# Kernel tuning notes

Hardware: AMD Instinct MI355X
Metric: run time of the kernel (lower is better)

Reference implementation:

```python
import jax, jax.numpy as jnp
import numpy as np
from functools import reduce

N_QUBITS = 6
DIM = 2 ** N_QUBITS  # 64

# PauliZ expectation signs per wire: zsign[j, q] = +1 if bit q of basis state j is 0 else -1
# PennyLane convention: wire 0 is the most-significant bit.
_ZSIGN = jnp.asarray(1.0 - 2.0 * ((np.arange(DIM)[:, None] >> (N_QUBITS - 1 - np.arange(N_QUBITS))[None, :]) & 1), dtype=jnp.float32)  # [64, 6]

def _cnot_perm(c, t):
    # permutation p with new_state[j] = old_state[p[j]] for CNOT(control=c, target=t)
    idx = np.arange(DIM)
    cbit = (idx >> (N_QUBITS - 1 - c)) & 1
    return idx ^ (cbit << (N_QUBITS - 1 - t))

def _ring_perm(r):
    # compose the ring of CNOTs: CNOT(w, (w+r)%n) for w = 0..n-1 applied in order
    total = np.arange(DIM)
    for w in range(N_QUBITS):
        total = total[_cnot_perm(w, (w + r) % N_QUBITS)]
    return total

_RING = {r: jnp.asarray(_ring_perm(r)) for r in (1, 2)}

def _rot(phi, theta, omega):
    # PennyLane Rot(phi, theta, omega) = RZ(omega) @ RY(theta) @ RZ(phi)
    c = jnp.cos(theta / 2.0)
    s = jnp.sin(theta / 2.0)
    em = jnp.exp(-0.5j * (phi + omega))
    ep = jnp.exp(0.5j * (phi - omega))
    return jnp.stack([jnp.stack([em * c, -ep * s]),
                      jnp.stack([jnp.conj(ep) * s, jnp.conj(em) * c])])

def _strongly_entangling(psi, theta):
    # theta: [L, N_QUBITS, 3]; psi: [B, 64] complex
    L = theta.shape[0]
    for l in range(L):
        mats = [_rot(theta[l, w, 0], theta[l, w, 1], theta[l, w, 2]) for w in range(N_QUBITS)]
        U = reduce(jnp.kron, mats)  # [64, 64]; wire 0 = most significant, matches kron order
        psi = psi @ U.T
        r = l % (N_QUBITS - 1) + 1  # PennyLane default ranges
        psi = psi[:, _RING[r]]
    return psi

def setup_inputs() -> dict:
    key = jax.random.key(0)
    ks = jax.random.split(key, 12)
    B, D, H, NW = 131072, 64, 64, 5
    return {
        'x': jax.random.normal(ks[0], (B, D), dtype=jnp.float32),
        'W1': jax.random.normal(ks[1], (H, D), dtype=jnp.float32) * 0.1,
        'b1': jnp.zeros((H,), dtype=jnp.float32),
        'ln_g': jnp.ones((H,), dtype=jnp.float32),
        'ln_b': jnp.zeros((H,), dtype=jnp.float32),
        'W2': jax.random.normal(ks[2], (N_QUBITS, H), dtype=jnp.float32) * 0.1,
        'b2': jnp.zeros((N_QUBITS,), dtype=jnp.float32),
        'theta_shared': jax.random.normal(ks[3], (2, N_QUBITS, 3), dtype=jnp.float32) * 0.1,
        'theta_task': jax.random.normal(ks[4], (1, N_QUBITS, 3), dtype=jnp.float32) * 0.1,
        'Wc': jax.random.normal(ks[5], (NW, N_QUBITS), dtype=jnp.float32) * 0.1,
        'bc': jnp.zeros((NW,), dtype=jnp.float32),
    }

def reference(x, W1, b1, ln_g, ln_b, W2, b2, theta_shared, theta_task, Wc, bc):
    # --- encoder: Linear -> ReLU -> LayerNorm -> Linear -> Tanh ---
    h = jax.nn.relu(x @ W1.T + b1)
    mu = h.mean(-1, keepdims=True)
    var = ((h - mu) ** 2).mean(-1, keepdims=True)
    h = (h - mu) / jnp.sqrt(var + 1e-5) * ln_g + ln_b
    z = jnp.tanh(h @ W2.T + b2)  # [B, 6], in [-1, 1]
    # --- amplitude prep: RY(pi * z_q) on |0> per qubit -> product state ---
    half = (jnp.pi * z) / 2.0
    vec = jnp.stack([jnp.cos(half), jnp.sin(half)], axis=-1)  # [B, 6, 2]
    psi = vec[:, 0]
    for q in range(1, N_QUBITS):
        psi = (psi[:, :, None] * vec[:, q][:, None, :]).reshape(psi.shape[0], -1)
    psi = psi.astype(jnp.complex64)  # [B, 64]
    # --- VQC layers ---
    psi = _strongly_entangling(psi, theta_shared)
    psi = _strongly_entangling(psi, theta_task)
    # --- PauliZ expectation per wire ---
    probs = (psi * jnp.conj(psi)).real  # [B, 64]
    q_out = probs @ _ZSIGN  # [B, 6]
    # --- linear classifier ---
    return q_out @ Wc.T + bc
```

## Files before the change

### kernel.cpp

```cpp
#include <hip/hip_runtime.h>
#include <utility>

#define NQ 6
#define DIM 64

typedef float v2f __attribute__((ext_vector_type(2)));

namespace {

constexpr int ring_entry(int r, int i) {
    int idx = i;
    for (int w = NQ - 1; w >= 0; --w) {
        int c = w;
        int t = (w + r) % NQ;
        int cbit = (idx >> (NQ - 1 - c)) & 1;
        idx ^= cbit << (NQ - 1 - t);
    }
    return idx;
}

constexpr int Mc(int L, int i) {
    if (L == 1) return ring_entry(1, i);
    if (L == 2) return ring_entry(1, ring_entry(2, i));
    if (L == 3) return ring_entry(1, ring_entry(2, ring_entry(1, i)));
    return i;
}

constexpr int Minv(int L, int p) {
    for (int i = 0; i < DIM; ++i) if (Mc(L, i) == p) return i;
    return -1;
}

}

__device__ __forceinline__ float swap1(float v) {
    return __int_as_float(__builtin_amdgcn_mov_dpp(__float_as_int(v), 0xB1, 0xF, 0xF, true));
}
__device__ __forceinline__ v2f swap1v(v2f v) {
    v2f r; r.x = swap1(v.x); r.y = swap1(v.y); return r;
}
__device__ __forceinline__ v2f nsw(v2f v) {
    v2f r; r.x = -v.y; r.y = v.x; return r;
}


template<int LY, int W, int d, int... Ls>
__device__ __forceinline__ void wire_inlane(v2f* sv,
        float A0r, float A0i, float B0r, float B0i,
        float A1r, float A1i, float B1r, float B1i,
        std::integer_sequence<int, Ls...>) {
    (([&] {
        if constexpr (Ls < (Ls ^ d)) {
            constexpr int la = Ls, lb = Ls ^ d;
            constexpr int ra = (Minv(LY, la) >> (5 - W)) & 1;
            constexpr int rb = (Minv(LY, lb) >> (5 - W)) & 1;
            const float cAar = ra ? A1r : A0r, cAai = ra ? A1i : A0i;
            const float cBar = ra ? B1r : B0r, cBai = ra ? B1i : B0i;
            const float cAbr = rb ? A1r : A0r, cAbi = rb ? A1i : A0i;
            const float cBbr = rb ? B1r : B0r, cBbi = rb ? B1i : B0i;
            const v2f ma = sv[la], mb = sv[lb];
            const v2f na = nsw(ma), nb = nsw(mb);
            sv[la] = cAar*ma + cAai*na + cBar*mb + cBai*nb;
            sv[lb] = cAbr*mb + cAbi*nb + cBbr*ma + cBbi*na;
        }
    }()), ...);
}

template<int LY, int W, int... Ls>
__device__ __forceinline__ void wire_cross0(v2f* sv,
        float A0r, float A0i, float B0r, float B0i,
        float A1r, float A1i, float B1r, float B1i,
        std::integer_sequence<int, Ls...>) {
    (([&] {
        constexpr int r = (Minv(LY, Ls) >> (5 - W)) & 1;
        const float cAr = r ? A1r : A0r, cAi = r ? A1i : A0i;
        const float cBr = r ? B1r : B0r, cBi = r ? B1i : B0i;
        const v2f m = sv[Ls];
        const v2f t = swap1v(m);
        sv[Ls] = cAr*m + cAi*nsw(m) + cBr*t + cBi*nsw(t);
    }()), ...);
}

template<int LY, int W, int d, int... Ls>
__device__ __forceinline__ void wire_crossd(v2f* sv,
        float A0r, float A0i, float B0r, float B0i,
        float A1r, float A1i, float B1r, float B1i,
        std::integer_sequence<int, Ls...>) {
    (([&] {
        if constexpr (Ls < (Ls ^ d)) {
            constexpr int la = Ls, lb = Ls ^ d;
            constexpr int ra = (Minv(LY, la) >> (5 - W)) & 1;
            constexpr int rb = (Minv(LY, lb) >> (5 - W)) & 1;
            const float cAar = ra ? A1r : A0r, cAai = ra ? A1i : A0i;
            const float cBar = ra ? B1r : B0r, cBai = ra ? B1i : B0i;
            const float cAbr = rb ? A1r : A0r, cAbi = rb ? A1i : A0i;
            const float cBbr = rb ? B1r : B0r, cBbi = rb ? B1i : B0i;
            const v2f ma = sv[la], mb = sv[lb];
            const v2f ta = swap1v(mb);
            const v2f tb = swap1v(ma);
            sv[la] = cAar*ma + cAai*nsw(ma) + cBar*ta + cBai*nsw(ta);
            sv[lb] = cAbr*mb + cAbi*nsw(mb) + cBbr*tb + cBbi*nsw(tb);
        }
    }()), ...);
}

template<int LY, int W>
__device__ __forceinline__ void wire_apply(v2f* sv,
        const float* __restrict__ g, bool par) {
    constexpr int D = Mc(LY, 1 << (5 - W));
    constexpr bool cross = (D >> 5) & 1;
    constexpr int d = D & 31;
    constexpr bool cpar = (Minv(LY, 32) >> (5 - W)) & 1;

    float A0r, A0i, B0r, B0i, A1r, A1i, B1r, B1i;
    if constexpr (cpar) {
        A0r = par ? g[6] : g[0];  A0i = par ? g[7] : g[1];
        B0r = par ? g[4] : g[2];  B0i = par ? g[5] : g[3];
        A1r = par ? g[0] : g[6];  A1i = par ? g[1] : g[7];
        B1r = par ? g[2] : g[4];  B1i = par ? g[3] : g[5];
    } else {
        A0r = g[0]; A0i = g[1]; B0r = g[2]; B0i = g[3];
        A1r = g[6]; A1i = g[7]; B1r = g[4]; B1i = g[5];
    }
    if constexpr (!cross) {
        wire_inlane<LY, W, d>(sv, A0r, A0i, B0r, B0i, A1r, A1i, B1r, B1i,
                              std::make_integer_sequence<int, 32>{});
    } else if constexpr (d == 0) {
        wire_cross0<LY, W>(sv, A0r, A0i, B0r, B0i, A1r, A1i, B1r, B1i,
                           std::make_integer_sequence<int, 32>{});
    } else {
        wire_crossd<LY, W, d>(sv, A0r, A0i, B0r, B0i, A1r, A1i, B1r, B1i,
                              std::make_integer_sequence<int, 32>{});
    }
}

template<int LY>
__device__ __forceinline__ void layer_apply(v2f* sv,
        const float* __restrict__ g, bool par) {
    wire_apply<LY, 0>(sv, g,      par);
    wire_apply<LY, 1>(sv, g + 8,  par);
    wire_apply<LY, 2>(sv, g + 16, par);
    wire_apply<LY, 3>(sv, g + 24, par);
    wire_apply<LY, 4>(sv, g + 32, par);
    wire_apply<LY, 5>(sv, g + 40, par);
}

template<int... Ls>
__device__ __forceinline__ void readout_impl(const v2f* sv, float* q,
                                             std::integer_sequence<int, Ls...>) {
    (([&] {
        constexpr int iv = Minv(3, Ls);
        const float pb = fmaf(sv[Ls].x, sv[Ls].x, sv[Ls].y * sv[Ls].y);
        q[0] += ((iv >> 5) & 1) ? -pb : pb;
        q[1] += ((iv >> 4) & 1) ? -pb : pb;
        q[2] += ((iv >> 3) & 1) ? -pb : pb;
        q[3] += ((iv >> 2) & 1) ? -pb : pb;
        q[4] += ((iv >> 1) & 1) ? -pb : pb;
        q[5] += ( iv       & 1) ? -pb : pb;
    }()), ...);
}

__device__ __forceinline__ void compute_gates6(const float* __restrict__ th, float* g) {
#pragma unroll
    for (int w = 0; w < NQ; ++w) {
        const float phi = th[w*3+0], theta = th[w*3+1], omega = th[w*3+2];
        float s, c, sa, ca, sb, cb;
        __sincosf(0.5f * theta, &s, &c);
        __sincosf(0.5f * (phi + omega), &sa, &ca);
        __sincosf(0.5f * (phi - omega), &sb, &cb);
        g[w*8+0] =  ca * c;  g[w*8+1] = -sa * c;
        g[w*8+2] = -cb * s;  g[w*8+3] = -sb * s;
        g[w*8+4] =  cb * s;  g[w*8+5] = -sb * s;
        g[w*8+6] =  ca * c;  g[w*8+7] =  sa * c;
    }
}

__global__ void setup_kernel(const float* __restrict__ th_s, const float* __restrict__ th_t,
                             const float* __restrict__ ln_g, const float* __restrict__ ln_b,
                             const float* __restrict__ W2, const float* __restrict__ b2,
                             float* __restrict__ ws) {
    const int t = threadIdx.x;
    if (t < 18) {
        const int l = t / 6, w = t % 6;
        const float* th = (l < 2) ? (th_s + (l * 6 + w) * 3) : (th_t + w * 3);
        const float phi = th[0], theta = th[1], omega = th[2];
        float s, c, sa, ca, sb, cb;
        sincosf(0.5f * theta, &s, &c);
        sincosf(0.5f * (phi + omega), &sa, &ca);
        sincosf(0.5f * (phi - omega), &sb, &cb);
        float* g = ws + t * 8;
        g[0] =  ca * c;  g[1] = -sa * c;
        g[2] = -cb * s;  g[3] = -sb * s;
        g[4] =  cb * s;  g[5] = -sb * s;
        g[6] =  ca * c;  g[7] =  sa * c;
    }
    if (t < 384) {
        const int j = t / 6, m = t % 6;
        ws[144 + t] = ln_g[j] * W2[m * 64 + j];
    }
    if (t < 6) {
        float c1 = 0.f, c2 = 0.f;
        for (int j = 0; j < 64; ++j) {
            c1 += ln_g[j] * W2[t * 64 + j];
            c2 += ln_b[j] * W2[t * 64 + j];
        }
        ws[528 + t] = c1;
        ws[534 + t] = c2 + b2[t];
    }
}

template<bool USE_WS>
__global__ __launch_bounds__(256, 4)
void qmaml_kernel(
    const float* __restrict__ x,  const float* __restrict__ W1, const float* __restrict__ b1,
    const float* __restrict__ ln_g, const float* __restrict__ ln_b,
    const float* __restrict__ W2, const float* __restrict__ b2,
    const float* __restrict__ th_s, const float* __restrict__ th_t,
    const float* __restrict__ Wc, const float* __restrict__ bc,
    const float* __restrict__ ws, float* __restrict__ out, int nrows) {

    __shared__ float4 wl[1024];
    {
        const float4* wg = (const float4*)W1;
        const int tid = threadIdx.x;
#pragma unroll
        for (int k = 0; k < 4; ++k) wl[tid + (k << 8)] = wg[tid + (k << 8)];
    }
    __syncthreads();

    const int t   = blockIdx.x * 256 + threadIdx.x;
    const int row = t >> 1;
    const bool par = t & 1;
    if (row >= nrows) return;

    float4 xv[8];
    const float4* xp = (const float4*)(x + (long)row * 64 + par * 32);
#pragma unroll
    for (int k = 0; k < 8; ++k) xv[k] = xp[k];
    v2f xl[16];
#pragma unroll
    for (int k = 0; k < 8; ++k) {
        xl[2*k].x   = xv[k].x; xl[2*k].y   = xv[k].y;
        xl[2*k+1].x = xv[k].z; xl[2*k+1].y = xv[k].w;
    }

    v2f A2[3]; A2[0] = 0.f; A2[1] = 0.f; A2[2] = 0.f;
    float A[6]  = {0.f, 0.f, 0.f, 0.f, 0.f, 0.f};
    float C1[6] = {0.f, 0.f, 0.f, 0.f, 0.f, 0.f};
    float C2[6] = {0.f, 0.f, 0.f, 0.f, 0.f, 0.f};
    float s = 0.f, s2 = 0.f;

    const float4* whalf = &wl[par * 8];
#pragma unroll 2
    for (int j = 0; j < 64; ++j) {
        const float4* wr = whalf + j * 16;
        v2f pa; pa = 0.f;
        v2f pb; pb = 0.f;
#pragma unroll
        for (int k = 0; k < 8; k += 2) {
            const float4 a4 = wr[k];
            const float4 b4 = wr[k + 1];
            v2f w0; w0.x = a4.x; w0.y = a4.y;
            v2f w1; w1.x = a4.z; w1.y = a4.w;
            v2f w2v; w2v.x = b4.x; w2v.y = b4.y;
            v2f w3; w3.x = b4.z; w3.y = b4.w;
            pa = w0  * xl[2*k]     + pa;
            pb = w1  * xl[2*k + 1] + pb;
            pa = w2v * xl[2*k + 2] + pa;
            pb = w3  * xl[2*k + 3] + pb;
        }
        const v2f pv = pa + pb;
        const float p   = pv.x + pv.y;
        const float tot = p + swap1(p);
        const float acc = fmaxf(tot + b1[j], 0.f);
        s += acc; s2 = fmaf(acc, acc, s2);
        if constexpr (USE_WS) {
            const v2f* Gt2 = (const v2f*)(ws + 144 + j * 6);
            A2[0] = acc * Gt2[0] + A2[0];
            A2[1] = acc * Gt2[1] + A2[1];
            A2[2] = acc * Gt2[2] + A2[2];
        } else {
            const float gj = ln_g[j], bj = ln_b[j];
#pragma unroll
            for (int m = 0; m < 6; ++m) {
                const float w2 = W2[m * 64 + j];
                const float gw = gj * w2;
                A[m]  = fmaf(acc, gw, A[m]);
                C1[m] += gw;
                C2[m] = fmaf(bj, w2, C2[m]);
            }
        }
    }
    if constexpr (USE_WS) {
        A[0] = A2[0].x; A[1] = A2[0].y; A[2] = A2[1].x;
        A[3] = A2[1].y; A[4] = A2[2].x; A[5] = A2[2].y;
    }

    const float mu  = s  * (1.f / 64.f);
    const float var = s2 * (1.f / 64.f) - mu * mu;
    const float inv = rsqrtf(var + 1e-5f);

    float vc[6], vsn[6];
#pragma unroll
    for (int m = 0; m < 6; ++m) {
        float c1v, c2v;
        if constexpr (USE_WS) { c1v = ws[528 + m]; c2v = ws[534 + m]; }
        else                  { c1v = C1[m];       c2v = C2[m] + b2[m]; }
        const float zp = inv * (A[m] - mu * c1v) + c2v;
        const float e  = __expf(2.f * zp);
        const float z  = 1.f - 2.f / (e + 1.f);
        const float half = 1.57079632679f * z;
        vsn[m] = __sinf(half);
        vc[m]  = __cosf(half);
    }

    float gf[48];
    const float* g0;
    if constexpr (USE_WS) g0 = ws;
    else { compute_gates6(th_s, gf); g0 = gf; }

    v2f sv[32];
    {
        const float a0r = par ? (g0[4]*vc[0] + g0[6]*vsn[0]) : (g0[0]*vc[0] + g0[2]*vsn[0]);
        const float a0i = par ? (g0[5]*vc[0] + g0[7]*vsn[0]) : (g0[1]*vc[0] + g0[3]*vsn[0]);
        v2f ga1; ga1.x = g0[8]  * vc[1] + g0[10] * vsn[1];
                 ga1.y = g0[9]  * vc[1] + g0[11] * vsn[1];
        v2f gb1; gb1.x = g0[12] * vc[1] + g0[14] * vsn[1];
                 gb1.y = g0[13] * vc[1] + g0[15] * vsn[1];
        sv[0] = a0r * ga1 + a0i * nsw(ga1);
        sv[1] = a0r * gb1 + a0i * nsw(gb1);
    }
    {
        v2f ya; ya.x = g0[16]*vc[2] + g0[18]*vsn[2]; ya.y = g0[17]*vc[2] + g0[19]*vsn[2];
        v2f yb; yb.x = g0[20]*vc[2] + g0[22]*vsn[2]; yb.y = g0[21]*vc[2] + g0[23]*vsn[2];
        const v2f nya = nsw(ya), nyb = nsw(yb);
#pragma unroll
        for (int k = 3; k >= 0; --k) {
            const v2f h = sv[k >> 1];
            const v2f y  = (k & 1) ? yb  : ya;
            const v2f ny = (k & 1) ? nyb : nya;
            sv[k] = h.x * y + h.y * ny;
        }
    }
    {
        v2f ya; ya.x = g0[24]*vc[3] + g0[26]*vsn[3]; ya.y = g0[25]*vc[3] + g0[27]*vsn[3];
        v2f yb; yb.x = g0[28]*vc[3] + g0[30]*vsn[3]; yb.y = g0[29]*vc[3] + g0[31]*vsn[3];
        const v2f nya = nsw(ya), nyb = nsw(yb);
#pragma unroll
        for (int k = 7; k >= 0; --k) {
            const v2f h = sv[k >> 1];
            const v2f y  = (k & 1) ? yb  : ya;
            const v2f ny = (k & 1) ? nyb : nya;
            sv[k] = h.x * y + h.y * ny;
        }
    }
    {
        v2f ya; ya.x = g0[32]*vc[4] + g0[34]*vsn[4]; ya.y = g0[33]*vc[4] + g0[35]*vsn[4];
        v2f yb; yb.x = g0[36]*vc[4] + g0[38]*vsn[4]; yb.y = g0[37]*vc[4] + g0[39]*vsn[4];
        const v2f nya = nsw(ya), nyb = nsw(yb);
#pragma unroll
        for (int k = 15; k >= 0; --k) {
            const v2f h = sv[k >> 1];
            const v2f y  = (k & 1) ? yb  : ya;
            const v2f ny = (k & 1) ? nyb : nya;
            sv[k] = h.x * y + h.y * ny;
        }
    }
    {
        v2f ya; ya.x = g0[40]*vc[5] + g0[42]*vsn[5]; ya.y = g0[41]*vc[5] + g0[43]*vsn[5];
        v2f yb; yb.x = g0[44]*vc[5] + g0[46]*vsn[5]; yb.y = g0[45]*vc[5] + g0[47]*vsn[5];
        const v2f nya = nsw(ya), nyb = nsw(yb);
#pragma unroll
        for (int k = 31; k >= 0; --k) {
            const v2f h = sv[k >> 1];
            const v2f y  = (k & 1) ? yb  : ya;
            const v2f ny = (k & 1) ? nyb : nya;
            sv[k] = h.x * y + h.y * ny;
        }
    }

    if constexpr (USE_WS) {
        layer_apply<1>(sv, ws + 48, par);
        layer_apply<2>(sv, ws + 96, par);
    } else {
        compute_gates6(th_s + 18, gf);
        layer_apply<1>(sv, gf, par);
        compute_gates6(th_t, gf);
        layer_apply<2>(sv, gf, par);
    }

    float q[6] = {0.f, 0.f, 0.f, 0.f, 0.f, 0.f};
    readout_impl(sv, q, std::make_integer_sequence<int, 32>{});

    const float pm = par ? -1.f : 1.f;
    constexpr int invC = Minv(3, 32);
#pragma unroll
    for (int w = 0; w < 6; ++w) {
        float tq = q[w];
        if ((invC >> (5 - w)) & 1) tq *= pm;
        q[w] = tq + swap1(tq);
    }

    float o[5];
#pragma unroll
    for (int n = 0; n < 5; ++n) {
        float v = bc[n];
#pragma unroll
        for (int w = 0; w < 6; ++w) v = fmaf(q[w], Wc[n * 6 + w], v);
        o[n] = v;
    }
    float* orow = out + (long)row * 5;
    if (!par) { orow[0] = o[0]; orow[1] = o[1]; orow[2] = o[2]; }
    else      { orow[3] = o[3]; orow[4] = o[4]; }
}

extern "C" void kernel_launch(void* const* d_in, const int* in_sizes, int n_in,
                              void* d_out, int out_size, void* d_ws, size_t ws_size,
                              hipStream_t stream) {
    const float* x   = (const float*)d_in[0];
    const float* W1  = (const float*)d_in[1];
    const float* b1  = (const float*)d_in[2];
    const float* lng = (const float*)d_in[3];
    const float* lnb = (const float*)d_in[4];
    const float* W2  = (const float*)d_in[5];
    const float* b2  = (const float*)d_in[6];
    const float* ths = (const float*)d_in[7];
    const float* tht = (const float*)d_in[8];
    const float* Wc  = (const float*)d_in[9];
    const float* bc  = (const float*)d_in[10];
    float* out = (float*)d_out;
    float* ws  = (float*)d_ws;

    const int nrows = in_sizes[0] / 64;
    const int nthreads = nrows * 2;
    const int grid = (nthreads + 255) / 256;

    if (ws_size >= 540 * sizeof(float)) {
        setup_kernel<<<1, 384, 0, stream>>>(ths, tht, lng, lnb, W2, b2, ws);
        qmaml_kernel<true><<<grid, 256, 0, stream>>>(x, W1, b1, lng, lnb, W2, b2,
                                                     ths, tht, Wc, bc, ws, out, nrows);
    } else {
        qmaml_kernel<false><<<grid, 256, 0, stream>>>(x, W1, b1, lng, lnb, W2, b2,
                                                      ths, tht, Wc, bc, nullptr, out, nrows);
    }
}
```

Measured before the change: 140.6 us.

## Split hidden units across thread pair instead of input dimension

Measured after the change: 147.1 us. 1.05x slower.

```diff
diff --git a/kernel.cpp b/kernel.cpp
--- a/kernel.cpp
+++ b/kernel.cpp
@@ -178,7 +178,7 @@
 __global__ void setup_kernel(const float* __restrict__ th_s, const float* __restrict__ th_t,
                              const float* __restrict__ ln_g, const float* __restrict__ ln_b,
                              const float* __restrict__ W2, const float* __restrict__ b2,
-                             float* __restrict__ ws) {
+                             const float* __restrict__ b1, float* __restrict__ ws) {
     const int t = threadIdx.x;
     if (t < 18) {
         const int l = t / 6, w = t % 6;
@@ -196,7 +196,11 @@
     }
     if (t < 384) {
         const int j = t / 6, m = t % 6;
-        ws[144 + t] = ln_g[j] * W2[m * 64 + j];
+        ws[144 + j * 8 + m] = ln_g[j] * W2[m * 64 + j];
+    }
+    if (t < 64) {
+        ws[144 + t * 8 + 6] = b1[t];
+        ws[144 + t * 8 + 7] = 0.f;
     }
     if (t < 6) {
         float c1 = 0.f, c2 = 0.f;
@@ -204,8 +208,8 @@
             c1 += ln_g[j] * W2[t * 64 + j];
             c2 += ln_b[j] * W2[t * 64 + j];
         }
-        ws[528 + t] = c1;
-        ws[534 + t] = c2 + b2[t];
+        ws[656 + t] = c1;
+        ws[662 + t] = c2 + b2[t];
     }
 }
 
@@ -233,15 +237,15 @@
     const bool par = t & 1;
     if (row >= nrows) return;
 
-    float4 xv[8];
-    const float4* xp = (const float4*)(x + (long)row * 64 + par * 32);
-#pragma unroll
-    for (int k = 0; k < 8; ++k) xv[k] = xp[k];
-    v2f xl[16];
-#pragma unroll
-    for (int k = 0; k < 8; ++k) {
-        xl[2*k].x   = xv[k].x; xl[2*k].y   = xv[k].y;
-        xl[2*k+1].x = xv[k].z; xl[2*k+1].y = xv[k].w;
+    v2f xl[32];
+    {
+        const float4* xp = (const float4*)(x + (long)row * 64);
+#pragma unroll
+        for (int k = 0; k < 16; ++k) {
+            const float4 v = xp[k];
+            xl[2*k].x   = v.x; xl[2*k].y   = v.y;
+            xl[2*k+1].x = v.z; xl[2*k+1].y = v.w;
+        }
     }
 
     v2f A2[3]; A2[0] = 0.f; A2[1] = 0.f; A2[2] = 0.f;
@@ -250,36 +254,43 @@
     float C2[6] = {0.f, 0.f, 0.f, 0.f, 0.f, 0.f};
     float s = 0.f, s2 = 0.f;
 
-    const float4* whalf = &wl[par * 8];
+    const int jbase = par << 5;
 #pragma unroll 2
-    for (int j = 0; j < 64; ++j) {
-        const float4* wr = whalf + j * 16;
+    for (int jj = 0; jj < 32; ++jj) {
+        const int j = jbase + jj;
+        const float4* wr = &wl[j * 16];
         v2f pa; pa = 0.f;
         v2f pb; pb = 0.f;
-#pragma unroll
-        for (int k = 0; k < 8; k += 2) {
-            const float4 a4 = wr[k];
-            const float4 b4 = wr[k + 1];
-            v2f w0; w0.x = a4.x; w0.y = a4.y;
-            v2f w1; w1.x = a4.z; w1.y = a4.w;
-            v2f w2v; w2v.x = b4.x; w2v.y = b4.y;
-            v2f w3; w3.x = b4.z; w3.y = b4.w;
-            pa = w0  * xl[2*k]     + pa;
-            pb = w1  * xl[2*k + 1] + pb;
-            pa = w2v * xl[2*k + 2] + pa;
-            pb = w3  * xl[2*k + 3] + pb;
-        }
-        const v2f pv = pa + pb;
-        const float p   = pv.x + pv.y;
-        const float tot = p + swap1(p);
-        const float acc = fmaxf(tot + b1[j], 0.f);
-        s += acc; s2 = fmaf(acc, acc, s2);
+        v2f pc; pc = 0.f;
+        v2f pd; pd = 0.f;
+#pragma unroll
+        for (int k = 0; k < 4; ++k) {
+            const float4 a4 = wr[4*k+0];
+            const float4 b4 = wr[4*k+1];
+            const float4 c4 = wr[4*k+2];
+            const float4 d4 = wr[4*k+3];
+            v2f t0; t0.x = a4.x; t0.y = a4.y; pa = t0 * xl[8*k+0] + pa;
+            v2f t1; t1.x = a4.z; t1.y = a4.w; pb = t1 * xl[8*k+1] + pb;
+            v2f t2; t2.x = b4.x; t2.y = b4.y; pc = t2 * xl[8*k+2] + pc;
+            v2f t3; t3.x = b4.z; t3.y = b4.w; pd = t3 * xl[8*k+3] + pd;
+            v2f t4; t4.x = c4.x; t4.y = c4.y; pa = t4 * xl[8*k+4] + pa;
+            v2f t5; t5.x = c4.z; t5.y = c4.w; pb = t5 * xl[8*k+5] + pb;
+            v2f t6; t6.x = d4.x; t6.y = d4.y; pc = t6 * xl[8*k+6] + pc;
+            v2f t7; t7.x = d4.z; t7.y = d4.w; pd = t7 * xl[8*k+7] + pd;
+        }
+        const v2f pv = (pa + pb) + (pc + pd);
+        const float tot = pv.x + pv.y;
         if constexpr (USE_WS) {
-            const v2f* Gt2 = (const v2f*)(ws + 144 + j * 6);
-            A2[0] = acc * Gt2[0] + A2[0];
-            A2[1] = acc * Gt2[1] + A2[1];
-            A2[2] = acc * Gt2[2] + A2[2];
+            const v2f* Gt = (const v2f*)(ws + 144 + j * 8);
+            const v2f g3 = Gt[3];
+            const float acc = fmaxf(tot + g3.x, 0.f);
+            s += acc; s2 = fmaf(acc, acc, s2);
+            A2[0] = acc * Gt[0] + A2[0];
+            A2[1] = acc * Gt[1] + A2[1];
+            A2[2] = acc * Gt[2] + A2[2];
         } else {
+            const float acc = fmaxf(tot + b1[j], 0.f);
+            s += acc; s2 = fmaf(acc, acc, s2);
             const float gj = ln_g[j], bj = ln_b[j];
 #pragma unroll
             for (int m = 0; m < 6; ++m) {
@@ -291,9 +302,21 @@
             }
         }
     }
+    s  = s  + swap1(s);
+    s2 = s2 + swap1(s2);
     if constexpr (USE_WS) {
+        A2[0] = A2[0] + swap1v(A2[0]);
+        A2[1] = A2[1] + swap1v(A2[1]);
+        A2[2] = A2[2] + swap1v(A2[2]);
         A[0] = A2[0].x; A[1] = A2[0].y; A[2] = A2[1].x;
         A[3] = A2[1].y; A[4] = A2[2].x; A[5] = A2[2].y;
+    } else {
+#pragma unroll
+        for (int m = 0; m < 6; ++m) {
+            A[m]  = A[m]  + swap1(A[m]);
+            C1[m] = C1[m] + swap1(C1[m]);
+            C2[m] = C2[m] + swap1(C2[m]);
+        }
     }
 
     const float mu  = s  * (1.f / 64.f);
@@ -304,7 +327,7 @@
 #pragma unroll
     for (int m = 0; m < 6; ++m) {
         float c1v, c2v;
-        if constexpr (USE_WS) { c1v = ws[528 + m]; c2v = ws[534 + m]; }
+        if constexpr (USE_WS) { c1v = ws[656 + m]; c2v = ws[662 + m]; }
         else                  { c1v = C1[m];       c2v = C2[m] + b2[m]; }
         const float zp = inv * (A[m] - mu * c1v) + c2v;
         const float e  = __expf(2.f * zp);
@@ -435,8 +458,8 @@
     const int nthreads = nrows * 2;
     const int grid = (nthreads + 255) / 256;
 
-    if (ws_size >= 540 * sizeof(float)) {
-        setup_kernel<<<1, 384, 0, stream>>>(ths, tht, lng, lnb, W2, b2, ws);
+    if (ws_size >= 668 * sizeof(float)) {
+        setup_kernel<<<1, 384, 0, stream>>>(ths, tht, lng, lnb, W2, b2, b1, ws);
         qmaml_kernel<true><<<grid, 256, 0, stream>>>(x, W1, b1, lng, lnb, W2, b2,
                                                      ths, tht, Wc, bc, ws, out, nrows);
     } else {
```
